# Optimization experiments

Measured on AMD Instinct MI355X. Metric: run time of the kernel, lower is better.

The kernel has to match this reference:

```python
import jax, jax.numpy as jnp
import numpy as np

RC = 5.2                                   # radial cutoff Rcr
ETA_R = np.array([16.0], dtype=np.float32)
SHF_R = (0.9 + 0.26875 * np.arange(16)).astype(np.float32)
NUM_SPECIES = 4                             # len(vocabulary)


def setup_inputs() -> dict:
    key = jax.random.key(0)
    kp, ks = jax.random.split(key)
    B, N = 64, 256
    # random positions in a 12 A box -> realistic distance matrices
    pos = jax.random.uniform(kp, (B, N, 3), jnp.float32, 0.0, 12.0)
    diff = pos[:, :, None, :] - pos[:, None, :, :]
    d = jnp.sqrt(jnp.sum(diff * diff, axis=-1) + 1e-12)
    d = d * (1.0 - jnp.eye(N, dtype=jnp.float32))  # zero self-distance
    species = jax.random.randint(ks, (B, N), 1, NUM_SPECIES + 1, jnp.int32)
    return {"distance_matrices_batch": d, "num_species_batch": species}


def reference(distance_matrices_batch, num_species_batch):
    d = distance_matrices_batch                      # [B, N, N]
    eta = jnp.asarray(ETA_R)
    shf = jnp.asarray(SHF_R)
    # cartesian product of (EtaR, ShfR), P = len(EtaR)*len(ShfR)
    eta_p = jnp.repeat(eta, shf.shape[0])            # [P]
    shf_p = jnp.tile(shf, eta.shape[0])              # [P]

    mask = (d < RC) & (d != 0.0)                     # [B, N, N]
    fc = 0.5 * jnp.cos(jnp.pi * d / RC) + 0.5        # ANAKIN cutoff fn
    # Gaussian radial terms, masked to the cutoff neighborhood
    terms = jnp.exp(-eta_p * (d[..., None] - shf_p) ** 2) * fc[..., None]  # [B,N,N,P]
    terms = jnp.where(mask[..., None], terms, jnp.zeros((), terms.dtype))

    # one-hot of neighbor species (IDs are 1-based)
    oh = jax.nn.one_hot(num_species_batch - 1, NUM_SPECIES, dtype=terms.dtype)  # [B,N,S]
    # scatter-sum over neighbors j, bucketed by species of j
    GR = jnp.einsum('bijp,bjs->bisp', terms, oh)     # [B, N, S, P]
    B, N = d.shape[0], d.shape[1]
    return GR.reshape(B, N, NUM_SPECIES * terms.shape[-1])  # [B, N, S*P]
```

## Files before the change

### kernel.cpp

```cpp
#include <hip/hip_runtime.h>
#include <stdint.h>


static __device__ __forceinline__ int mbcnt64(uint64_t m) {
    int lo = __builtin_amdgcn_mbcnt_lo((uint32_t)m, 0u);
    return __builtin_amdgcn_mbcnt_hi((uint32_t)(m >> 32), lo);
}

typedef float vfloat2 __attribute__((ext_vector_type(2)));
typedef float vfloat4 __attribute__((ext_vector_type(4)));

#define KNEG (-23.083120654223414f)

__global__ __launch_bounds__(256, 8) void aev_kernel(
    const float* __restrict__ dmat,
    const int* __restrict__ species,
    float* __restrict__ out)
{
    __shared__ alignas(16) float2 comp[8][256];
    __shared__ alignas(16) int    pos[256];
    __shared__ alignas(16) float  red[8][64];
    __shared__ int cntm[4][4];

    const int tid  = threadIdx.x;
    const int w    = tid >> 6;
    const int lane = tid & 63;
    const int blk  = (int)blockIdx.x;
    const int row0 = blk * 8 + w * 2;
    const int b    = blk >> 5;

    const vfloat4 qa = __builtin_nontemporal_load(
        (const vfloat4*)(dmat + ((size_t)row0 << 8)) + lane);
    const vfloat4 qb = __builtin_nontemporal_load(
        (const vfloat4*)(dmat + ((size_t)(row0 + 1) << 8)) + lane);

    int sj = species[(b << 8) + tid] - 1;
    sj = (sj < 0) ? 0 : ((sj > 3) ? 3 : sj);
    const uint64_t bs0 = __ballot((sj & 1) != 0);
    const uint64_t bs1 = __ballot((sj & 2) != 0);
    const uint64_t m0 = ~bs0 & ~bs1, m1 = bs0 & ~bs1;
    const uint64_t m2 = ~bs0 &  bs1, m3 = bs0 &  bs1;
    if (lane == 0) {
        cntm[w][0] = __popcll(m0); cntm[w][1] = __popcll(m1);
        cntm[w][2] = __popcll(m2); cntm[w][3] = __popcll(m3);
    }
    uint64_t msel = m0;
    msel = (sj == 1) ? m1 : msel;
    msel = (sj == 2) ? m2 : msel;
    msel = (sj == 3) ? m3 : msel;
    const int rank = mbcnt64(msel);
    __syncthreads();

    int seg[5];
    seg[0] = 0;
    #pragma unroll
    for (int s = 0; s < 4; ++s)
        seg[s + 1] = __builtin_amdgcn_readfirstlane(
            seg[s] + cntm[0][s] + cntm[1][s] + cntm[2][s] + cntm[3][s]);
    {
        int base = seg[0];
        base = (sj == 1) ? seg[1] : base;
        base = (sj == 2) ? seg[2] : base;
        base = (sj == 3) ? seg[3] : base;
        int wadd = 0;
        #pragma unroll
        for (int w2 = 0; w2 < 3; ++w2) wadd += (w2 < w) ? cntm[w2][sj] : 0;
        pos[tid] = base + wadd + rank;
    }
    __syncthreads();

    {
        const int4 p4 = *(const int4*)&pos[4 * lane];
        const int   pp[4] = {p4.x, p4.y, p4.z, p4.w};
        const float da[4] = {qa.x, qa.y, qa.z, qa.w};
        const float db[4] = {qb.x, qb.y, qb.z, qb.w};
        const float NINF = -__builtin_inff();
        const int lr = w * 2;
        #pragma unroll
        for (int e = 0; e < 4; ++e) {
            const float dd = da[e];
            const bool  v  = (dd < 5.2f) && (dd != 0.0f);
            const float x  = v ? dd : 2.6f;
            const float fc = 0.5f * __builtin_amdgcn_cosf(x * (0.5f / 5.2f)) + 0.5f;
            const float cA = __builtin_fmaf(KNEG * x, x, __builtin_amdgcn_logf(fc));
            comp[lr][pp[e]] = make_float2(v ? cA : NINF, v ? (-2.0f * KNEG) * x : 0.0f);
        }
        #pragma unroll
        for (int e = 0; e < 4; ++e) {
            const float dd = db[e];
            const bool  v  = (dd < 5.2f) && (dd != 0.0f);
            const float x  = v ? dd : 2.6f;
            const float fc = 0.5f * __builtin_amdgcn_cosf(x * (0.5f / 5.2f)) + 0.5f;
            const float cA = __builtin_fmaf(KNEG * x, x, __builtin_amdgcn_logf(fc));
            comp[lr + 1][pp[e]] = make_float2(v ? cA : NINF, v ? (-2.0f * KNEG) * x : 0.0f);
        }
    }
    __syncthreads();

    const int g  = lane >> 4;
    const int qp = (lane >> 2) & 3;
    const int sp = lane & 3;
    const int lr = w * 2;

    const float shf0 = 0.9f + 0.26875f * (float)(4 * g);

    const int sbeg = (sp == 0) ? seg[0] : (sp == 1) ? seg[1] : (sp == 2) ? seg[2] : seg[3];
    const int send = (sp == 0) ? seg[1] : (sp == 1) ? seg[2] : (sp == 2) ? seg[3] : seg[4];
    int maxLen = seg[1] - seg[0];
    maxLen = (seg[2] - seg[1] > maxLen) ? seg[2] - seg[1] : maxLen;
    maxLen = (seg[3] - seg[2] > maxLen) ? seg[3] - seg[2] : maxLen;
    maxLen = (seg[4] - seg[3] > maxLen) ? seg[4] - seg[3] : maxLen;
    const int nIt = __builtin_amdgcn_readfirstlane((maxLen + 3) >> 2);

    const float NINF = -__builtin_inff();
    float a0x = 0.f, a0y = 0.f, a0z = 0.f, a0w = 0.f;
    float a1x = 0.f, a1y = 0.f, a1z = 0.f, a1w = 0.f;
    for (int m = 0; m < nIt; ++m) {
        const int k  = sbeg + qp + 4 * m;
        const int kc = (k < 255) ? k : 255;
        const bool live = (k < send);
        const float2 cR0 = comp[lr][kc];
        const float2 cR1 = comp[lr + 1][kc];
        const float A0 = live ? cR0.x : NINF;
        const float A1 = live ? cR1.x : NINF;
        #pragma unroll
        for (int t = 0; t < 4; ++t) {
            const float sh = shf0 + 0.26875f * (float)t;
            const float kp = KNEG * sh * sh;
            const float e0 = __builtin_amdgcn_exp2f(__builtin_fmaf(cR0.y, sh, A0) + kp);
            const float e1 = __builtin_amdgcn_exp2f(__builtin_fmaf(cR1.y, sh, A1) + kp);
            if (t == 0) { a0x += e0; a1x += e1; }
            if (t == 1) { a0y += e0; a1y += e1; }
            if (t == 2) { a0z += e0; a1z += e1; }
            if (t == 3) { a0w += e0; a1w += e1; }
        }
    }

    #pragma unroll
    for (int d = 4; d <= 8; d <<= 1) {
        a0x += __shfl_xor(a0x, d, 64); a0y += __shfl_xor(a0y, d, 64);
        a0z += __shfl_xor(a0z, d, 64); a0w += __shfl_xor(a0w, d, 64);
        a1x += __shfl_xor(a1x, d, 64); a1y += __shfl_xor(a1y, d, 64);
        a1z += __shfl_xor(a1z, d, 64); a1w += __shfl_xor(a1w, d, 64);
    }

    if (qp == 0) {
        float4* r0 = (float4*)&red[lr][(sp << 4) + (g << 2)];
        float4* r1 = (float4*)&red[lr + 1][(sp << 4) + (g << 2)];
        *r0 = make_float4(a0x, a0y, a0z, a0w);
        *r1 = make_float4(a1x, a1y, a1z, a1w);
    }

    {
        const int r  = lane >> 5;
        const int c2 = lane & 31;
        const float2 rv = ((const float2*)&red[lr + r][0])[c2];
        vfloat2 nv; nv.x = rv.x; nv.y = rv.y;
        vfloat2* dst = (vfloat2*)&out[((size_t)(row0 + r) << 6) + (size_t)(c2 * 2)];
        __builtin_nontemporal_store(nv, dst);
    }
}

extern "C" void kernel_launch(void* const* d_in, const int* in_sizes, int n_in,
                              void* d_out, int out_size, void* d_ws, size_t ws_size,
                              hipStream_t stream) {
    const float* dmat  = (const float*)d_in[0];
    const int* species = (const int*)d_in[1];
    float* o           = (float*)d_out;
    const int B = in_sizes[1] >> 8;
    aev_kernel<<<dim3(B * 32), 256, 0, stream>>>(dmat, species, o);
}
```

Before: 75.41 us.

## Compact in-cutoff neighbors per row and use exp recurrence across shifts

The species bucketing is rebuilt per wave with ballots over each row's own in-cutoff mask, so each row's compacted list holds only valid neighbors sorted by species. This drops the shared pos array, the cntm counts and two block barriers. The four Gaussian shifts per thread now come from two exp2 calls plus multiplies, using a geometric recurrence in place of four exponentials. The loop length now scales with the in-cutoff neighbor count rather than all 256 atoms. In exchange the recurrence adds some floating-point error, and the ballot bookkeeping adds integer work.

```diff
diff --git a/kernel.cpp b/kernel.cpp
--- a/kernel.cpp
+++ b/kernel.cpp
@@ -10,17 +10,16 @@
 typedef float vfloat2 __attribute__((ext_vector_type(2)));
 typedef float vfloat4 __attribute__((ext_vector_type(4)));
 
-#define KNEG (-23.083120654223414f)
+#define KNEG  (-23.083120654223414f)
+#define DELTA (0.26875f)
 
 __global__ __launch_bounds__(256, 8) void aev_kernel(
     const float* __restrict__ dmat,
     const int* __restrict__ species,
     float* __restrict__ out)
 {
-    __shared__ alignas(16) float2 comp[8][256];
-    __shared__ alignas(16) int    pos[256];
+    __shared__ alignas(16) float2 comp[8][260];
     __shared__ alignas(16) float  red[8][64];
-    __shared__ int cntm[4][4];
 
     const int tid  = threadIdx.x;
     const int w    = tid >> 6;
@@ -28,112 +27,126 @@
     const int blk  = (int)blockIdx.x;
     const int row0 = blk * 8 + w * 2;
     const int b    = blk >> 5;
+    const int lr   = w * 2;
 
     const vfloat4 qa = __builtin_nontemporal_load(
         (const vfloat4*)(dmat + ((size_t)row0 << 8)) + lane);
     const vfloat4 qb = __builtin_nontemporal_load(
         (const vfloat4*)(dmat + ((size_t)(row0 + 1) << 8)) + lane);
 
-    int sj = species[(b << 8) + tid] - 1;
-    sj = (sj < 0) ? 0 : ((sj > 3) ? 3 : sj);
-    const uint64_t bs0 = __ballot((sj & 1) != 0);
-    const uint64_t bs1 = __ballot((sj & 2) != 0);
-    const uint64_t m0 = ~bs0 & ~bs1, m1 = bs0 & ~bs1;
-    const uint64_t m2 = ~bs0 &  bs1, m3 = bs0 &  bs1;
-    if (lane == 0) {
-        cntm[w][0] = __popcll(m0); cntm[w][1] = __popcll(m1);
-        cntm[w][2] = __popcll(m2); cntm[w][3] = __popcll(m3);
+    const int4 s4 = ((const int4*)(species + (b << 8)))[lane];
+    int sv[4] = {s4.x - 1, s4.y - 1, s4.z - 1, s4.w - 1};
+    #pragma unroll
+    for (int e = 0; e < 4; ++e) sv[e] = (sv[e] < 0) ? 0 : ((sv[e] > 3) ? 3 : sv[e]);
+
+    uint64_t sm[4][4];
+    #pragma unroll
+    for (int e = 0; e < 4; ++e) {
+        const uint64_t c0 = __ballot((sv[e] & 1) != 0);
+        const uint64_t c1 = __ballot((sv[e] & 2) != 0);
+        sm[e][0] = ~c0 & ~c1; sm[e][1] = c0 & ~c1;
+        sm[e][2] = ~c0 &  c1; sm[e][3] = c0 &  c1;
     }
-    uint64_t msel = m0;
-    msel = (sj == 1) ? m1 : msel;
-    msel = (sj == 2) ? m2 : msel;
-    msel = (sj == 3) ? m3 : msel;
-    const int rank = mbcnt64(msel);
-    __syncthreads();
 
-    int seg[5];
-    seg[0] = 0;
+    const float dv0[4] = {qa.x, qa.y, qa.z, qa.w};
+    const float dv1[4] = {qb.x, qb.y, qb.z, qb.w};
+    const float NINF = -__builtin_inff();
+    int sb[2][5];
+
     #pragma unroll
-    for (int s = 0; s < 4; ++s)
-        seg[s + 1] = __builtin_amdgcn_readfirstlane(
-            seg[s] + cntm[0][s] + cntm[1][s] + cntm[2][s] + cntm[3][s]);
-    {
-        int base = seg[0];
-        base = (sj == 1) ? seg[1] : base;
-        base = (sj == 2) ? seg[2] : base;
-        base = (sj == 3) ? seg[3] : base;
-        int wadd = 0;
-        #pragma unroll
-        for (int w2 = 0; w2 < 3; ++w2) wadd += (w2 < w) ? cntm[w2][sj] : 0;
-        pos[tid] = base + wadd + rank;
-    }
-    __syncthreads();
-
-    {
-        const int4 p4 = *(const int4*)&pos[4 * lane];
-        const int   pp[4] = {p4.x, p4.y, p4.z, p4.w};
-        const float da[4] = {qa.x, qa.y, qa.z, qa.w};
-        const float db[4] = {qb.x, qb.y, qb.z, qb.w};
-        const float NINF = -__builtin_inff();
-        const int lr = w * 2;
+    for (int r = 0; r < 2; ++r) {
+        uint64_t bvE[4];
+        int cnt[4] = {0, 0, 0, 0};
         #pragma unroll
         for (int e = 0; e < 4; ++e) {
-            const float dd = da[e];
+            const float dd = (r == 0) ? dv0[e] : dv1[e];
+            bvE[e] = __ballot((dd < 5.2f) && (dd != 0.0f));
+            #pragma unroll
+            for (int s = 0; s < 4; ++s) cnt[s] += __popcll(bvE[e] & sm[e][s]);
+        }
+        sb[r][0] = 0;
+        #pragma unroll
+        for (int s = 0; s < 4; ++s) sb[r][s + 1] = sb[r][s] + cnt[s];
+
+        int run[4] = {sb[r][0], sb[r][1], sb[r][2], sb[r][3]};
+        #pragma unroll
+        for (int e = 0; e < 4; ++e) {
+            const float dd = (r == 0) ? dv0[e] : dv1[e];
             const bool  v  = (dd < 5.2f) && (dd != 0.0f);
             const float x  = v ? dd : 2.6f;
             const float fc = 0.5f * __builtin_amdgcn_cosf(x * (0.5f / 5.2f)) + 0.5f;
             const float cA = __builtin_fmaf(KNEG * x, x, __builtin_amdgcn_logf(fc));
-            comp[lr][pp[e]] = make_float2(v ? cA : NINF, v ? (-2.0f * KNEG) * x : 0.0f);
-        }
-        #pragma unroll
-        for (int e = 0; e < 4; ++e) {
-            const float dd = db[e];
-            const bool  v  = (dd < 5.2f) && (dd != 0.0f);
-            const float x  = v ? dd : 2.6f;
-            const float fc = 0.5f * __builtin_amdgcn_cosf(x * (0.5f / 5.2f)) + 0.5f;
-            const float cA = __builtin_fmaf(KNEG * x, x, __builtin_amdgcn_logf(fc));
-            comp[lr + 1][pp[e]] = make_float2(v ? cA : NINF, v ? (-2.0f * KNEG) * x : 0.0f);
+            const float cB = (-2.0f * KNEG) * x;
+            const int s = sv[e];
+            uint64_t msel = bvE[e] & sm[e][0];
+            msel = (s == 1) ? (bvE[e] & sm[e][1]) : msel;
+            msel = (s == 2) ? (bvE[e] & sm[e][2]) : msel;
+            msel = (s == 3) ? (bvE[e] & sm[e][3]) : msel;
+            int base = run[0];
+            base = (s == 1) ? run[1] : base;
+            base = (s == 2) ? run[2] : base;
+            base = (s == 3) ? run[3] : base;
+            const int slot0 = base + mbcnt64(msel);
+            const int slot  = (slot0 < 259) ? slot0 : 259;
+            if (v) comp[lr + r][slot] = make_float2(cA, cB);
+            #pragma unroll
+            for (int s2 = 0; s2 < 4; ++s2) run[s2] += __popcll(bvE[e] & sm[e][s2]);
         }
     }
-    __syncthreads();
 
     const int g  = lane >> 4;
     const int qp = (lane >> 2) & 3;
     const int sp = lane & 3;
-    const int lr = w * 2;
 
-    const float shf0 = 0.9f + 0.26875f * (float)(4 * g);
+    const float sh0 = 0.9f + DELTA * (float)(4 * g);
+    const float kp0 = KNEG * sh0 * sh0;
+    const float dc0 = KNEG * DELTA * (2.0f * sh0 + DELTA);
+    const float qc  = __builtin_amdgcn_exp2f(2.0f * KNEG * DELTA * DELTA);
 
-    const int sbeg = (sp == 0) ? seg[0] : (sp == 1) ? seg[1] : (sp == 2) ? seg[2] : seg[3];
-    const int send = (sp == 0) ? seg[1] : (sp == 1) ? seg[2] : (sp == 2) ? seg[3] : seg[4];
-    int maxLen = seg[1] - seg[0];
-    maxLen = (seg[2] - seg[1] > maxLen) ? seg[2] - seg[1] : maxLen;
-    maxLen = (seg[3] - seg[2] > maxLen) ? seg[3] - seg[2] : maxLen;
-    maxLen = (seg[4] - seg[3] > maxLen) ? seg[4] - seg[3] : maxLen;
-    const int nIt = __builtin_amdgcn_readfirstlane((maxLen + 3) >> 2);
+    const int sbeg0 = (sp == 0) ? sb[0][0] : (sp == 1) ? sb[0][1] : (sp == 2) ? sb[0][2] : sb[0][3];
+    const int send0 = (sp == 0) ? sb[0][1] : (sp == 1) ? sb[0][2] : (sp == 2) ? sb[0][3] : sb[0][4];
+    const int sbeg1 = (sp == 0) ? sb[1][0] : (sp == 1) ? sb[1][1] : (sp == 2) ? sb[1][2] : sb[1][3];
+    const int send1 = (sp == 0) ? sb[1][1] : (sp == 1) ? sb[1][2] : (sp == 2) ? sb[1][3] : sb[1][4];
 
-    const float NINF = -__builtin_inff();
+    int ml = 0;
+    #pragma unroll
+    for (int r = 0; r < 2; ++r)
+        #pragma unroll
+        for (int s = 0; s < 4; ++s) {
+            const int L = sb[r][s + 1] - sb[r][s];
+            ml = (L > ml) ? L : ml;
+        }
+    const int nIt = (ml + 3) >> 2;
+
     float a0x = 0.f, a0y = 0.f, a0z = 0.f, a0w = 0.f;
     float a1x = 0.f, a1y = 0.f, a1z = 0.f, a1w = 0.f;
     for (int m = 0; m < nIt; ++m) {
-        const int k  = sbeg + qp + 4 * m;
-        const int kc = (k < 255) ? k : 255;
-        const bool live = (k < send);
-        const float2 cR0 = comp[lr][kc];
-        const float2 cR1 = comp[lr + 1][kc];
-        const float A0 = live ? cR0.x : NINF;
-        const float A1 = live ? cR1.x : NINF;
-        #pragma unroll
-        for (int t = 0; t < 4; ++t) {
-            const float sh = shf0 + 0.26875f * (float)t;
-            const float kp = KNEG * sh * sh;
-            const float e0 = __builtin_amdgcn_exp2f(__builtin_fmaf(cR0.y, sh, A0) + kp);
-            const float e1 = __builtin_amdgcn_exp2f(__builtin_fmaf(cR1.y, sh, A1) + kp);
-            if (t == 0) { a0x += e0; a1x += e1; }
-            if (t == 1) { a0y += e0; a1y += e1; }
-            if (t == 2) { a0z += e0; a1z += e1; }
-            if (t == 3) { a0w += e0; a1w += e1; }
-        }
+        const int k0 = sbeg0 + qp + 4 * m;
+        const int k1 = sbeg1 + qp + 4 * m;
+        const int k0c = (k0 < 259) ? k0 : 259;
+        const int k1c = (k1 < 259) ? k1 : 259;
+        const float2 u0 = comp[lr][k0c];
+        const float2 u1 = comp[lr + 1][k1c];
+        const bool l0 = (k0 < send0);
+        const bool l1 = (k1 < send1);
+        const float A0 = l0 ? u0.x : NINF;
+        const float B0 = l0 ? u0.y : 0.0f;
+        const float A1 = l1 ? u1.x : NINF;
+        const float B1 = l1 ? u1.y : 0.0f;
+
+        float E0 = __builtin_amdgcn_exp2f(__builtin_fmaf(B0, sh0, A0) + kp0);
+        float T0 = __builtin_amdgcn_exp2f(__builtin_fmaf(DELTA, B0, dc0));
+        a0x += E0; E0 *= T0; T0 *= qc;
+        a0y += E0; E0 *= T0; T0 *= qc;
+        a0z += E0; E0 *= T0;
+        a0w += E0;
+
+        float E1 = __builtin_amdgcn_exp2f(__builtin_fmaf(B1, sh0, A1) + kp0);
+        float T1 = __builtin_amdgcn_exp2f(__builtin_fmaf(DELTA, B1, dc0));
+        a1x += E1; E1 *= T1; T1 *= qc;
+        a1y += E1; E1 *= T1; T1 *= qc;
+        a1z += E1; E1 *= T1;
+        a1w += E1;
     }
 
     #pragma unroll
```

New measurement: 96.45 us. 27.9% more time.
